# Performance work log

Measured on AMD Instinct MI355X. Metric: run time of the kernel, lower is better.

Reference implementation:

```python
import jax, jax.numpy as jnp
import numpy as np

K = 3
PAD = 1


def conv3x3(x, w):
    # x: [B,C,H,W], w: [O,C,3,3] -> [B,O,H,W], stride 1, pad 1, no bias
    return jax.lax.conv_general_dilated(
        x, w, window_strides=(1, 1), padding=((PAD, PAD), (PAD, PAD)),
        dimension_numbers=("NCHW", "OIHW", "NCHW"))


def bilinear_gather(x, py, px):
    """Zero-padded bilinear sampling (torchvision deform_conv2d semantics).
    x: [B,C,H,W]; py, px: [B,KK,H,W] absolute sampling coords.
    Returns [B,C,KK,H,W]."""
    B, C, H, W = x.shape
    KK = py.shape[1]
    y0 = jnp.floor(py)
    x0 = jnp.floor(px)
    wy1 = py - y0  # frac weights
    wx1 = px - x0
    wy0 = 1.0 - wy1
    wx0 = 1.0 - wx1
    x_flat = x.reshape(B, C, H * W)

    def corner(yi, xi, w):
        valid = (yi >= 0) & (yi <= H - 1) & (xi >= 0) & (xi <= W - 1)
        yc = jnp.clip(yi, 0, H - 1).astype(jnp.int32)
        xc = jnp.clip(xi, 0, W - 1).astype(jnp.int32)
        idx = (yc * W + xc).reshape(B, 1, KK * H * W)
        v = jnp.take_along_axis(x_flat, jnp.broadcast_to(idx, (B, C, KK * H * W)), axis=2)
        v = v.reshape(B, C, KK, H, W)
        return v * (w * valid.astype(x.dtype))[:, None]

    return (corner(y0, x0, wy0 * wx0) + corner(y0, x0 + 1.0, wy0 * wx1)
            + corner(y0 + 1.0, x0, wy1 * wx0) + corner(y0 + 1.0, x0 + 1.0, wy1 * wx1))


def deform_conv2d(x, offset, weight):
    """x: [B,C,H,W]; offset: [B,2*K*K,H,W] (dy,dx interleaved per tap, row-major);
    weight: [O,C,K,K]. stride 1, pad 1, dilation 1, 1 group, 1 offset group."""
    B, C, H, W = x.shape
    O = weight.shape[0]
    off = offset.reshape(B, K * K, 2, H, W)
    dy, dx = off[:, :, 0], off[:, :, 1]  # [B,9,H,W]
    ki, kj = jnp.meshgrid(jnp.arange(K, dtype=x.dtype), jnp.arange(K, dtype=x.dtype), indexing="ij")
    ki = ki.reshape(1, K * K, 1, 1)
    kj = kj.reshape(1, K * K, 1, 1)
    hh = jnp.arange(H, dtype=x.dtype).reshape(1, 1, H, 1)
    ww = jnp.arange(W, dtype=x.dtype).reshape(1, 1, 1, W)
    py = hh - PAD + ki + dy  # [B,9,H,W]
    px = ww - PAD + kj + dx
    sampled = bilinear_gather(x, py, px)  # [B,C,9,H,W]
    return jnp.einsum("bckhw,ock->bohw", sampled, weight.reshape(O, C, K * K))


def offset_estimator(x, w1, w2, w3):
    # channel-preserving bottleneck stand-in for Dynamic_offset_estimator
    h = jax.nn.relu(conv3x3(x, w1))
    h = jax.nn.relu(conv3x3(h, w2))
    return conv3x3(h, w3)


def setup_inputs() -> dict:
    key = jax.random.key(0)
    ks = jax.random.split(key, 7)
    B, C, H, W = 1, 768, 64, 64
    C2, CM = 2 * C, 192
    f32 = jnp.float32
    inp = {
        "input_features": jax.random.normal(ks[0], (B, C, H, W), dtype=f32),
        "reference_features": jax.random.normal(ks[1], (B, C, H, W), dtype=f32),
        "est_w1": jax.random.normal(ks[2], (CM, C2, K, K), dtype=f32) / np.sqrt(C2 * K * K),
        "est_w2": jax.random.normal(ks[3], (CM, CM, K, K), dtype=f32) / np.sqrt(CM * K * K),
        "est_w3": jax.random.normal(ks[4], (C2, CM, K, K), dtype=f32) / np.sqrt(CM * K * K),
        "offset_w": jax.random.normal(ks[5], (18, C2, K, K), dtype=f32) / np.sqrt(C2 * K * K),
        "deform_w": jax.random.normal(ks[6], (C, C, K, K), dtype=f32) / np.sqrt(C * K * K),
    }
    return inp


def reference(input_features, reference_features, est_w1, est_w2, est_w3, offset_w, deform_w):
    input_offset = jnp.concatenate([input_features, reference_features], axis=1)  # [B,2C,H,W]
    est = offset_estimator(input_offset, est_w1, est_w2, est_w3)  # [B,2C,H,W]
    offset = conv3x3(est, offset_w)  # [B,18,H,W]
    return deform_conv2d(reference_features, offset, deform_w)  # [B,C,H,W]
```

## Files before the change

kernel.cpp:

```cpp
#include <hip/hip_runtime.h>

#define HWPX 4096

typedef short s8v  __attribute__((ext_vector_type(8)));
typedef float f4v  __attribute__((ext_vector_type(4)));

__device__ inline unsigned short f2bf(float f) {
    unsigned u = __float_as_uint(f);
    return (unsigned short)((u + 0x7fffu + ((u >> 16) & 1u)) >> 16);
}
__device__ inline float bf2f(unsigned s) {
    return __uint_as_float(s << 16);
}

__global__ __launch_bounds__(256)
void tr_cat_k(const float* __restrict__ xa, const float* __restrict__ xb,
              short* __restrict__ xt)
{
    __shared__ __align__(16) short T[64 * 72];
    const int c0 = blockIdx.x * 64, p0 = blockIdx.y * 64, tid = threadIdx.x;
    for (int i = tid; i < 4096; i += 256) {
        int cl = i >> 6, pl = i & 63;
        int c = c0 + cl;
        float v = (c < 768) ? xa[(size_t)c * HWPX + p0 + pl]
                            : xb[(size_t)(c - 768) * HWPX + p0 + pl];
        T[pl * 72 + cl] = (short)f2bf(v);
    }
    __syncthreads();
    for (int i = tid; i < 512; i += 256) {
        int pl = i >> 3, part = i & 7;
        uint4 v = *(const uint4*)&T[pl * 72 + part * 8];
        *(uint4*)&xt[(size_t)(p0 + pl) * 1536 + c0 + part * 8] = v;
    }
}

__global__ __launch_bounds__(256)
void wpack_k(const float* __restrict__ src, short* __restrict__ dst,
             int Cin, int Cout, int S, int NB, int total)
{
    int i = blockIdx.x * 256 + threadIdx.x;
    if (i >= total) return;
    int e = i & 7, lane = (i >> 3) & 63;
    int lm = lane & 15, quad = lane >> 4;
    int rest = i >> 9;
    int f = rest % NB;
    int s = (rest / NB) % S;
    int g = rest / (NB * S);
    int cout = g * (NB * 16) + f * 16 + lm;
    int cb = s / 9, t = s % 9;
    int ch = cb * 32 + quad * 8 + e;
    dst[i] = (cout < Cout) ? (short)f2bf(src[((size_t)cout * Cin + ch) * 9 + t]) : 0;
}

__global__ __launch_bounds__(256, 4)
void convf_k(const short* __restrict__ Xt, int CinStr,
             const short* __restrict__ Wp, int S, int chunks,
             short* __restrict__ Out, int Cstr, int splitStride)
{
    __shared__ __align__(16) short sH[6 * 66 * 40];
    const int tid = threadIdx.x, lane = tid & 63, wv = tid >> 6;
    const int lm = lane & 15, quad = lane >> 4;
    const int r0 = blockIdx.x * 4;
    const int g  = blockIdx.y;
    const int cb0 = blockIdx.z * chunks;
    short* out = Out + (size_t)blockIdx.z * splitStride;

    f4v acc[4][2];
#pragma unroll
    for (int ma = 0; ma < 4; ++ma)
#pragma unroll
        for (int nb = 0; nb < 2; ++nb)
#pragma unroll
            for (int r = 0; r < 4; ++r) acc[ma][nb][r] = 0.f;

    for (int cc = 0; cc < chunks; ++cc) {
        const int cb = cb0 + cc;
        const short* wpB = Wp + ((size_t)(g * S + cb * 9) * 2) * 512 + lane * 8;
        s8v bb[2];
        bb[0] = *(const s8v*)&wpB[0];
        bb[1] = *(const s8v*)&wpB[512];

        for (int i = tid; i < 1584; i += 256) {
            int slot = i >> 2, part = i & 3;
            int hr = slot / 66, px = slot % 66;
            int gy = r0 - 1 + hr, gx = px - 1;
            uint4 v = {0, 0, 0, 0};
            if (gy >= 0 && gy < 64 && gx >= 0 && gx < 64)
                v = *(const uint4*)&Xt[(size_t)(gy * 64 + gx) * CinStr + cb * 32 + part * 8];
            *(uint4*)&sH[slot * 40 + part * 8] = v;
        }
        __syncthreads();

#pragma unroll
        for (int t = 0; t < 9; ++t) {
            const int ty = t / 3, tx = t % 3;
            s8v nb0 = *(const s8v*)&wpB[(size_t)((t + 1) * 2 + 0) * 512];
            s8v nb1 = *(const s8v*)&wpB[(size_t)((t + 1) * 2 + 1) * 512];
            s8v a[4];
#pragma unroll
            for (int ma = 0; ma < 4; ++ma)
                a[ma] = *(const s8v*)&sH[((wv + ty) * 66 + ma * 16 + lm + tx) * 40 + quad * 8];
#pragma unroll
            for (int ma = 0; ma < 4; ++ma) {
                acc[ma][0] = __builtin_amdgcn_mfma_f32_16x16x32_bf16(a[ma], bb[0], acc[ma][0], 0, 0, 0);
                acc[ma][1] = __builtin_amdgcn_mfma_f32_16x16x32_bf16(a[ma], bb[1], acc[ma][1], 0, 0, 0);
            }
            bb[0] = nb0; bb[1] = nb1;
        }
        __syncthreads();
    }

    const int py = (r0 + wv) * 64;
#pragma unroll
    for (int ma = 0; ma < 4; ++ma)
#pragma unroll
        for (int nb = 0; nb < 2; ++nb)
#pragma unroll
            for (int r = 0; r < 4; ++r)
                out[(size_t)(py + ma * 16 + quad * 4 + r) * Cstr + g * 32 + nb * 16 + lm]
                    = (short)f2bf(acc[ma][nb][r]);
}

__global__ __launch_bounds__(256)
void ep_sumb_k(const short* __restrict__ P, short* __restrict__ outb,
               int nsplit, size_t splitStride, int n8, int relu)
{
    int i = blockIdx.x * 256 + threadIdx.x;
    if (i >= n8) return;
    size_t base = (size_t)i * 8;
    float s[8];
#pragma unroll
    for (int j = 0; j < 8; ++j) s[j] = 0.f;
    for (int sp = 0; sp < nsplit; ++sp) {
        uint4 v = *(const uint4*)&P[sp * splitStride + base];
        s[0] += bf2f(v.x & 0xffffu); s[1] += bf2f(v.x >> 16);
        s[2] += bf2f(v.y & 0xffffu); s[3] += bf2f(v.y >> 16);
        s[4] += bf2f(v.z & 0xffffu); s[5] += bf2f(v.z >> 16);
        s[6] += bf2f(v.w & 0xffffu); s[7] += bf2f(v.w >> 16);
    }
    if (relu) {
#pragma unroll
        for (int j = 0; j < 8; ++j) s[j] = fmaxf(s[j], 0.f);
    }
    uint4 o;
    o.x = f2bf(s[0]) | ((unsigned)f2bf(s[1]) << 16);
    o.y = f2bf(s[2]) | ((unsigned)f2bf(s[3]) << 16);
    o.z = f2bf(s[4]) | ((unsigned)f2bf(s[5]) << 16);
    o.w = f2bf(s[6]) | ((unsigned)f2bf(s[7]) << 16);
    *(uint4*)&outb[base] = o;
}

__global__ __launch_bounds__(256)
void ep_offs_k(const short* __restrict__ P, float* __restrict__ offs)
{
    int i = blockIdx.x * 256 + threadIdx.x;
    if (i >= 18 * HWPX) return;
    int m = i >> 12, px = i & 4095;
    float s = 0.f;
    for (int sp = 0; sp < 16; ++sp)
        s += bf2f((unsigned short)P[((size_t)sp * HWPX + px) * 32 + m]);
    offs[i] = s;
}

__global__ __launch_bounds__(256)
void sample_k(const short* __restrict__ xcat, const float* __restrict__ offs,
              short* __restrict__ Smp)
{
    __shared__ int   s_mi[9][16][4];
    __shared__ float s_mw[9][16][4];
    const int tid = threadIdx.x;
    const int p0  = blockIdx.x * 16;
    const int gb  = blockIdx.y * 24;

    if (tid < 144) {
        int t = tid / 16, p = tid % 16;
        int pxg = p0 + p;
        int r = pxg >> 6, x = pxg & 63;
        float dy = offs[(size_t)(2 * t)     * HWPX + pxg];
        float dx = offs[(size_t)(2 * t + 1) * HWPX + pxg];
        float py  = (float)(r - 1 + t / 3) + dy;
        float pxf = (float)(x - 1 + t % 3) + dx;
        py  = fminf(fmaxf(py,  -1e6f), 1e6f);
        pxf = fminf(fmaxf(pxf, -1e6f), 1e6f);
        float y0f = floorf(py), x0f = floorf(pxf);
        float wy1 = py - y0f, wx1 = pxf - x0f;
        float wy0 = 1.f - wy1, wx0 = 1.f - wx1;
        bool vy0 = (y0f >=  0.f) && (y0f <= 63.f);
        bool vy1 = (y0f >= -1.f) && (y0f <= 62.f);
        bool vx0 = (x0f >=  0.f) && (x0f <= 63.f);
        bool vx1 = (x0f >= -1.f) && (x0f <= 62.f);
        int y0 = (int)fminf(fmaxf(y0f,       0.f), 63.f);
        int y1 = (int)fminf(fmaxf(y0f + 1.f, 0.f), 63.f);
        int x0 = (int)fminf(fmaxf(x0f,       0.f), 63.f);
        int x1 = (int)fminf(fmaxf(x0f + 1.f, 0.f), 63.f);
        s_mi[t][p][0] = y0 * 64 + x0;  s_mw[t][p][0] = (vy0 && vx0) ? wy0 * wx0 : 0.f;
        s_mi[t][p][1] = y0 * 64 + x1;  s_mw[t][p][1] = (vy0 && vx1) ? wy0 * wx1 : 0.f;
        s_mi[t][p][2] = y1 * 64 + x0;  s_mw[t][p][2] = (vy1 && vx0) ? wy1 * wx0 : 0.f;
        s_mi[t][p][3] = y1 * 64 + x1;  s_mw[t][p][3] = (vy1 && vx1) ? wy1 * wx1 : 0.f;
    }
    __syncthreads();

    for (int i = tid; i < 16 * 9 * 24; i += 256) {
        int p = i / 216, rest = i % 216;
        int t = rest / 24, g = gb + rest % 24;
        float a[8];
#pragma unroll
        for (int j = 0; j < 8; ++j) a[j] = 0.f;
#pragma unroll
        for (int c = 0; c < 4; ++c) {
            float w = s_mw[t][p][c];
            const short* src = xcat + (size_t)s_mi[t][p][c] * 1536 + 768 + g * 8;
            uint4 v = *(const uint4*)src;
            a[0] += w * bf2f(v.x & 0xffffu); a[1] += w * bf2f(v.x >> 16);
            a[2] += w * bf2f(v.y & 0xffffu); a[3] += w * bf2f(v.y >> 16);
            a[4] += w * bf2f(v.z & 0xffffu); a[5] += w * bf2f(v.z >> 16);
            a[6] += w * bf2f(v.w & 0xffffu); a[7] += w * bf2f(v.w >> 16);
        }
        uint4 o;
        o.x = f2bf(a[0]) | ((unsigned)f2bf(a[1]) << 16);
        o.y = f2bf(a[2]) | ((unsigned)f2bf(a[3]) << 16);
        o.z = f2bf(a[4]) | ((unsigned)f2bf(a[5]) << 16);
        o.w = f2bf(a[6]) | ((unsigned)f2bf(a[7]) << 16);
        int px = p0 + p;
        int pg = px >> 6, ma = (px >> 4) & 3, lmx = px & 15;
        int cb = g >> 2, qd = g & 3;
        size_t addr = ((((size_t)pg * 216 + cb * 9 + t) * 4 + ma) * 64 + qd * 16 + lmx) * 8;
        *(uint4*)&Smp[addr] = o;
    }
}

__global__ __launch_bounds__(256, 3)
void dgemm_k(const short* __restrict__ Ap, const short* __restrict__ Bp,
             short* __restrict__ P)
{
    const int tid = threadIdx.x, lane = tid & 63, wv = tid >> 6;
    const int lm = lane & 15, quad = lane >> 4;
    const int mg = blockIdx.y * 2 + (wv >> 1);
    const int pg = blockIdx.x * 2 + (wv & 1);
    const int s0 = blockIdx.z * 54;
    const short* ap = Ap + (((size_t)mg * 216 + s0) * 4 * 64 + lane) * 8;
    const short* bp = Bp + (((size_t)pg * 216 + s0) * 4 * 64 + lane) * 8;

    f4v acc[4][4];
#pragma unroll
    for (int ma = 0; ma < 4; ++ma)
#pragma unroll
        for (int nb = 0; nb < 4; ++nb)
#pragma unroll
            for (int r = 0; r < 4; ++r) acc[ma][nb][r] = 0.f;

    s8v a0[4], b0[4], a1[4], b1[4];
#pragma unroll
    for (int f = 0; f < 4; ++f) {
        a0[f] = *(const s8v*)&ap[(size_t)f * 512];
        b0[f] = *(const s8v*)&bp[(size_t)f * 512];
    }

    for (int s = 0; s < 54; s += 2) {
#pragma unroll
        for (int f = 0; f < 4; ++f) {
            a1[f] = *(const s8v*)&ap[(size_t)((s + 1) * 4 + f) * 512];
            b1[f] = *(const s8v*)&bp[(size_t)((s + 1) * 4 + f) * 512];
        }
#pragma unroll
        for (int ma = 0; ma < 4; ++ma)
#pragma unroll
            for (int nb = 0; nb < 4; ++nb)
                acc[ma][nb] = __builtin_amdgcn_mfma_f32_16x16x32_bf16(
                    a0[ma], b0[nb], acc[ma][nb], 0, 0, 0);
#pragma unroll
        for (int f = 0; f < 4; ++f) {
            a0[f] = *(const s8v*)&ap[(size_t)((s + 2) * 4 + f) * 512];
            b0[f] = *(const s8v*)&bp[(size_t)((s + 2) * 4 + f) * 512];
        }
#pragma unroll
        for (int ma = 0; ma < 4; ++ma)
#pragma unroll
            for (int nb = 0; nb < 4; ++nb)
                acc[ma][nb] = __builtin_amdgcn_mfma_f32_16x16x32_bf16(
                    a1[ma], b1[nb], acc[ma][nb], 0, 0, 0);
    }

    short* p = P + (size_t)blockIdx.z * 768 * HWPX;
#pragma unroll
    for (int ma = 0; ma < 4; ++ma)
#pragma unroll
        for (int nb = 0; nb < 4; ++nb)
#pragma unroll
            for (int r = 0; r < 4; ++r)
                p[(size_t)(mg * 64 + ma * 16 + quad * 4 + r) * HWPX
                  + pg * 64 + nb * 16 + lm] = (short)f2bf(acc[ma][nb][r]);
}

__global__ __launch_bounds__(256)
void ep_dg_k(const short* __restrict__ P, float* __restrict__ out)
{
    int i = blockIdx.x * 256 + threadIdx.x;
    if (i >= 768 * HWPX / 8) return;
    size_t base = (size_t)i * 8;
    float s[8];
#pragma unroll
    for (int j = 0; j < 8; ++j) s[j] = 0.f;
    for (int sp = 0; sp < 4; ++sp) {
        uint4 v = *(const uint4*)&P[(size_t)sp * 768 * HWPX + base];
        s[0] += bf2f(v.x & 0xffffu); s[1] += bf2f(v.x >> 16);
        s[2] += bf2f(v.y & 0xffffu); s[3] += bf2f(v.y >> 16);
        s[4] += bf2f(v.z & 0xffffu); s[5] += bf2f(v.z >> 16);
        s[6] += bf2f(v.w & 0xffffu); s[7] += bf2f(v.w >> 16);
    }
    float4 o0 = make_float4(s[0], s[1], s[2], s[3]);
    float4 o1 = make_float4(s[4], s[5], s[6], s[7]);
    *(float4*)&out[base]     = o0;
    *(float4*)&out[base + 4] = o1;
}

extern "C" void kernel_launch(void* const* d_in, const int* in_sizes, int n_in,
                              void* d_out, int out_size, void* d_ws, size_t ws_size,
                              hipStream_t stream)
{
    const float* x_in  = (const float*)d_in[0];
    const float* x_ref = (const float*)d_in[1];
    const float* w1    = (const float*)d_in[2];
    const float* w2    = (const float*)d_in[3];
    const float* w3    = (const float*)d_in[4];
    const float* ow    = (const float*)d_in[5];
    const float* dw    = (const float*)d_in[6];
    float* out = (float*)d_out;

    char* w = (char*)d_ws;
    size_t off = 0;
    auto carve = [&](size_t bytes) {
        void* p = w + off;
        off += (bytes + 255) & ~(size_t)255;
        return p;
    };
    short* xcat = (short*)carve((size_t)4096 * 1536 * 2);
    short* w1p  = (short*)carve((size_t)6 * 432 * 2 * 512 * 2);
    short* w2p  = (short*)carve((size_t)6 * 54 * 2 * 512 * 2);
    short* w3p  = (short*)carve((size_t)48 * 54 * 2 * 512 * 2);
    short* w4p  = (short*)carve((size_t)1 * 432 * 2 * 512 * 2);
    short* dwp  = (short*)carve((size_t)12 * 216 * 4 * 512 * 2);
    float* offs = (float*)carve((size_t)18 * 4096 * 4);
    short* Smp  = (short*)carve((size_t)4096 * 6912 * 2);
    char*  R    = (char*)carve((size_t)2 * 768 * 4096 * 4);
    short* rh1  = (short*)R;
    short* rh2  = (short*)(R + 1572864);
    short* Pb   = (short*)(R + 3145728);
    short* est  = (short*)(R + 3145728);
    short* Pb4  = (short*)(R + 15728640);
    short* Pdg  = (short*)R;

    tr_cat_k<<<dim3(24, 64), 256, 0, stream>>>(x_in, x_ref, xcat);
    {
        int t1 = 6 * 432 * 2 * 512;
        wpack_k<<<(t1 + 255) / 256, 256, 0, stream>>>(w1, w1p, 1536, 192, 432, 2, t1);
        int t2 = 6 * 54 * 2 * 512;
        wpack_k<<<(t2 + 255) / 256, 256, 0, stream>>>(w2, w2p, 192, 192, 54, 2, t2);
        int t3 = 48 * 54 * 2 * 512;
        wpack_k<<<(t3 + 255) / 256, 256, 0, stream>>>(w3, w3p, 192, 1536, 54, 2, t3);
        int t4 = 1 * 432 * 2 * 512;
        wpack_k<<<(t4 + 255) / 256, 256, 0, stream>>>(ow, w4p, 1536, 18, 432, 2, t4);
        int t5 = 12 * 216 * 4 * 512;
        wpack_k<<<(t5 + 255) / 256, 256, 0, stream>>>(dw, dwp, 768, 768, 216, 4, t5);
    }

    const int n8 = 4096 * 192 / 8;
    convf_k<<<dim3(16, 6, 12), 256, 0, stream>>>(xcat, 1536, w1p, 432, 4,
                                                 Pb, 192, 4096 * 192);
    ep_sumb_k<<<(n8 + 255) / 256, 256, 0, stream>>>(Pb, rh1, 12, (size_t)4096 * 192, n8, 1);
    convf_k<<<dim3(16, 6, 6), 256, 0, stream>>>(rh1, 192, w2p, 54, 1,
                                                Pb, 192, 4096 * 192);
    ep_sumb_k<<<(n8 + 255) / 256, 256, 0, stream>>>(Pb, rh2, 6, (size_t)4096 * 192, n8, 1);
    convf_k<<<dim3(16, 48, 1), 256, 0, stream>>>(rh2, 192, w3p, 54, 6,
                                                 est, 1536, 0);
    convf_k<<<dim3(16, 1, 16), 256, 0, stream>>>(est, 1536, w4p, 432, 3,
                                                 Pb4, 32, 4096 * 32);
    ep_offs_k<<<(18 * HWPX + 255) / 256, 256, 0, stream>>>(Pb4, offs);
    sample_k<<<dim3(256, 4), 256, 0, stream>>>(xcat, offs, Smp);
    dgemm_k<<<dim3(32, 6, 4), 256, 0, stream>>>(dwp, Smp, Pdg);
    ep_dg_k<<<(768 * HWPX / 8 + 255) / 256, 256, 0, stream>>>(Pdg, out);
}
```

Before: 355.5 us.

## Widen conv output tile to 64 channels, retune split-K, fuse weight packing

Templates the conv kernel on the number of 16-wide output-channel blocks and uses 4 blocks (64 channels) for the estimator convs, so each staged input halo tile in LDS is reused across more MFMAs. Split-K factors and grids are retuned per layer, conv3 becomes split-K with an extra reduction pass, and the offset conv is split 48 ways. The five weight-packing launches are merged into one kernel and the partial buffers move into the sampling workspace. The cost is more accumulator registers, which lowers the launch-bounds occupancy hint from 4 to 3, plus extra partial-sum traffic for conv3.

```diff
diff --git a/kernel.cpp b/kernel.cpp
--- a/kernel.cpp
+++ b/kernel.cpp
@@ -34,12 +34,9 @@
     }
 }
 
-__global__ __launch_bounds__(256)
-void wpack_k(const float* __restrict__ src, short* __restrict__ dst,
-             int Cin, int Cout, int S, int NB, int total)
-{
-    int i = blockIdx.x * 256 + threadIdx.x;
-    if (i >= total) return;
+__device__ inline void wpack1(const float* __restrict__ src, short* __restrict__ dst,
+                              int i, int Cin, int Cout, int S, int NB)
+{
     int e = i & 7, lane = (i >> 3) & 63;
     int lm = lane & 15, quad = lane >> 4;
     int rest = i >> 9;
@@ -52,7 +49,30 @@
     dst[i] = (cout < Cout) ? (short)f2bf(src[((size_t)cout * Cin + ch) * 9 + t]) : 0;
 }
 
-__global__ __launch_bounds__(256, 4)
+#define C1 2654208
+#define C2 2985984
+#define C3 5640192
+#define C4 6082560
+#define C5 11390976
+
+__global__ __launch_bounds__(256)
+void wpack_all_k(const float* __restrict__ s1, const float* __restrict__ s2,
+                 const float* __restrict__ s3, const float* __restrict__ s4,
+                 const float* __restrict__ s5,
+                 short* __restrict__ d1, short* __restrict__ d2,
+                 short* __restrict__ d3, short* __restrict__ d4,
+                 short* __restrict__ d5)
+{
+    int i = blockIdx.x * 256 + threadIdx.x;
+    if (i < C1)      wpack1(s1, d1, i,      1536, 192,  432, 4);
+    else if (i < C2) wpack1(s2, d2, i - C1, 192,  192,  54,  4);
+    else if (i < C3) wpack1(s3, d3, i - C2, 192,  1536, 54,  4);
+    else if (i < C4) wpack1(s4, d4, i - C3, 1536, 18,   432, 2);
+    else if (i < C5) wpack1(s5, d5, i - C4, 768,  768,  216, 4);
+}
+
+template<int NB>
+__global__ __launch_bounds__(256, 3)
 void convf_k(const short* __restrict__ Xt, int CinStr,
              const short* __restrict__ Wp, int S, int chunks,
              short* __restrict__ Out, int Cstr, int splitStride)
@@ -65,20 +85,21 @@
     const int cb0 = blockIdx.z * chunks;
     short* out = Out + (size_t)blockIdx.z * splitStride;
 
-    f4v acc[4][2];
+    f4v acc[4][NB];
 #pragma unroll
     for (int ma = 0; ma < 4; ++ma)
 #pragma unroll
-        for (int nb = 0; nb < 2; ++nb)
+        for (int nb = 0; nb < NB; ++nb)
 #pragma unroll
             for (int r = 0; r < 4; ++r) acc[ma][nb][r] = 0.f;
 
     for (int cc = 0; cc < chunks; ++cc) {
         const int cb = cb0 + cc;
-        const short* wpB = Wp + ((size_t)(g * S + cb * 9) * 2) * 512 + lane * 8;
-        s8v bb[2];
-        bb[0] = *(const s8v*)&wpB[0];
-        bb[1] = *(const s8v*)&wpB[512];
+        const short* wpB = Wp + ((size_t)(g * S + cb * 9) * NB) * 512 + lane * 8;
+        s8v bb[NB];
+#pragma unroll
+        for (int f = 0; f < NB; ++f)
+            bb[f] = *(const s8v*)&wpB[(size_t)f * 512];
 
         for (int i = tid; i < 1584; i += 256) {
             int slot = i >> 2, part = i & 3;
@@ -94,18 +115,22 @@
 #pragma unroll
         for (int t = 0; t < 9; ++t) {
             const int ty = t / 3, tx = t % 3;
-            s8v nb0 = *(const s8v*)&wpB[(size_t)((t + 1) * 2 + 0) * 512];
-            s8v nb1 = *(const s8v*)&wpB[(size_t)((t + 1) * 2 + 1) * 512];
+            s8v nxt[NB];
+#pragma unroll
+            for (int f = 0; f < NB; ++f)
+                nxt[f] = *(const s8v*)&wpB[(size_t)((t + 1) * NB + f) * 512];
             s8v a[4];
 #pragma unroll
             for (int ma = 0; ma < 4; ++ma)
                 a[ma] = *(const s8v*)&sH[((wv + ty) * 66 + ma * 16 + lm + tx) * 40 + quad * 8];
 #pragma unroll
-            for (int ma = 0; ma < 4; ++ma) {
-                acc[ma][0] = __builtin_amdgcn_mfma_f32_16x16x32_bf16(a[ma], bb[0], acc[ma][0], 0, 0, 0);
-                acc[ma][1] = __builtin_amdgcn_mfma_f32_16x16x32_bf16(a[ma], bb[1], acc[ma][1], 0, 0, 0);
-            }
-            bb[0] = nb0; bb[1] = nb1;
+            for (int ma = 0; ma < 4; ++ma)
+#pragma unroll
+                for (int nb = 0; nb < NB; ++nb)
+                    acc[ma][nb] = __builtin_amdgcn_mfma_f32_16x16x32_bf16(
+                        a[ma], bb[nb], acc[ma][nb], 0, 0, 0);
+#pragma unroll
+            for (int f = 0; f < NB; ++f) bb[f] = nxt[f];
         }
         __syncthreads();
     }
@@ -114,11 +139,11 @@
 #pragma unroll
     for (int ma = 0; ma < 4; ++ma)
 #pragma unroll
-        for (int nb = 0; nb < 2; ++nb)
+        for (int nb = 0; nb < NB; ++nb)
 #pragma unroll
             for (int r = 0; r < 4; ++r)
-                out[(size_t)(py + ma * 16 + quad * 4 + r) * Cstr + g * 32 + nb * 16 + lm]
-                    = (short)f2bf(acc[ma][nb][r]);
+                out[(size_t)(py + ma * 16 + quad * 4 + r) * Cstr
+                    + g * (NB * 16) + nb * 16 + lm] = (short)f2bf(acc[ma][nb][r]);
 }
 
 __global__ __launch_bounds__(256)
@@ -151,13 +176,13 @@
 }
 
 __global__ __launch_bounds__(256)
-void ep_offs_k(const short* __restrict__ P, float* __restrict__ offs)
+void ep_offs_k(const short* __restrict__ P, float* __restrict__ offs, int nsplit)
 {
     int i = blockIdx.x * 256 + threadIdx.x;
     if (i >= 18 * HWPX) return;
     int m = i >> 12, px = i & 4095;
     float s = 0.f;
-    for (int sp = 0; sp < 16; ++sp)
+    for (int sp = 0; sp < nsplit; ++sp)
         s += bf2f((unsigned short)P[((size_t)sp * HWPX + px) * 32 + m]);
     offs[i] = s;
 }
@@ -335,47 +360,40 @@
         return p;
     };
     short* xcat = (short*)carve((size_t)4096 * 1536 * 2);
-    short* w1p  = (short*)carve((size_t)6 * 432 * 2 * 512 * 2);
-    short* w2p  = (short*)carve((size_t)6 * 54 * 2 * 512 * 2);
-    short* w3p  = (short*)carve((size_t)48 * 54 * 2 * 512 * 2);
-    short* w4p  = (short*)carve((size_t)1 * 432 * 2 * 512 * 2);
-    short* dwp  = (short*)carve((size_t)12 * 216 * 4 * 512 * 2);
+    short* w1p  = (short*)carve((size_t)C1 * 2);
+    short* w2p  = (short*)carve((size_t)(C2 - C1) * 2);
+    short* w3p  = (short*)carve((size_t)(C3 - C2) * 2);
+    short* w4p  = (short*)carve((size_t)(C4 - C3) * 2);
+    short* dwp  = (short*)carve((size_t)(C5 - C4) * 2);
     float* offs = (float*)carve((size_t)18 * 4096 * 4);
     short* Smp  = (short*)carve((size_t)4096 * 6912 * 2);
     char*  R    = (char*)carve((size_t)2 * 768 * 4096 * 4);
     short* rh1  = (short*)R;
     short* rh2  = (short*)(R + 1572864);
-    short* Pb   = (short*)(R + 3145728);
     short* est  = (short*)(R + 3145728);
-    short* Pb4  = (short*)(R + 15728640);
+    short* Pcv  = Smp;
     short* Pdg  = (short*)R;
 
     tr_cat_k<<<dim3(24, 64), 256, 0, stream>>>(x_in, x_ref, xcat);
+    wpack_all_k<<<(C5 + 255) / 256, 256, 0, stream>>>(w1, w2, w3, ow, dw,
+                                                      w1p, w2p, w3p, w4p, dwp);
+
+    const int n8 = 4096 * 192 / 8;
+    convf_k<4><<<dim3(16, 3, 16), 256, 0, stream>>>(xcat, 1536, w1p, 432, 3,
+                                                    Pcv, 192, 4096 * 192);
+    ep_sumb_k<<<(n8 + 255) / 256, 256, 0, stream>>>(Pcv, rh1, 16, (size_t)4096 * 192, n8, 1);
+    convf_k<4><<<dim3(16, 3, 6), 256, 0, stream>>>(rh1, 192, w2p, 54, 1,
+                                                   Pcv, 192, 4096 * 192);
+    ep_sumb_k<<<(n8 + 255) / 256, 256, 0, stream>>>(Pcv, rh2, 6, (size_t)4096 * 192, n8, 1);
+    convf_k<4><<<dim3(16, 24, 2), 256, 0, stream>>>(rh2, 192, w3p, 54, 3,
+                                                    Pcv, 1536, 4096 * 1536);
     {
-        int t1 = 6 * 432 * 2 * 512;
-        wpack_k<<<(t1 + 255) / 256, 256, 0, stream>>>(w1, w1p, 1536, 192, 432, 2, t1);
-        int t2 = 6 * 54 * 2 * 512;
-        wpack_k<<<(t2 + 255) / 256, 256, 0, stream>>>(w2, w2p, 192, 192, 54, 2, t2);
-        int t3 = 48 * 54 * 2 * 512;
-        wpack_k<<<(t3 + 255) / 256, 256, 0, stream>>>(w3, w3p, 192, 1536, 54, 2, t3);
-        int t4 = 1 * 432 * 2 * 512;
-        wpack_k<<<(t4 + 255) / 256, 256, 0, stream>>>(ow, w4p, 1536, 18, 432, 2, t4);
-        int t5 = 12 * 216 * 4 * 512;
-        wpack_k<<<(t5 + 255) / 256, 256, 0, stream>>>(dw, dwp, 768, 768, 216, 4, t5);
-    }
-
-    const int n8 = 4096 * 192 / 8;
-    convf_k<<<dim3(16, 6, 12), 256, 0, stream>>>(xcat, 1536, w1p, 432, 4,
-                                                 Pb, 192, 4096 * 192);
-    ep_sumb_k<<<(n8 + 255) / 256, 256, 0, stream>>>(Pb, rh1, 12, (size_t)4096 * 192, n8, 1);
-    convf_k<<<dim3(16, 6, 6), 256, 0, stream>>>(rh1, 192, w2p, 54, 1,
-                                                Pb, 192, 4096 * 192);
-    ep_sumb_k<<<(n8 + 255) / 256, 256, 0, stream>>>(Pb, rh2, 6, (size_t)4096 * 192, n8, 1);
-    convf_k<<<dim3(16, 48, 1), 256, 0, stream>>>(rh2, 192, w3p, 54, 6,
-                                                 est, 1536, 0);
-    convf_k<<<dim3(16, 1, 16), 256, 0, stream>>>(est, 1536, w4p, 432, 3,
-                                                 Pb4, 32, 4096 * 32);
-    ep_offs_k<<<(18 * HWPX + 255) / 256, 256, 0, stream>>>(Pb4, offs);
+        const int n8c3 = 4096 * 1536 / 8;
+        ep_sumb_k<<<(n8c3 + 255) / 256, 256, 0, stream>>>(Pcv, est, 2, (size_t)4096 * 1536, n8c3, 0);
+    }
+    convf_k<2><<<dim3(16, 1, 48), 256, 0, stream>>>(est, 1536, w4p, 432, 1,
+                                                    Pcv, 32, 4096 * 32);
+    ep_offs_k<<<(18 * HWPX + 255) / 256, 256, 0, stream>>>(Pcv, offs, 48);
     sample_k<<<dim3(256, 4), 256, 0, stream>>>(xcat, offs, Smp);
     dgemm_k<<<dim3(32, 6, 4), 256, 0, stream>>>(dwp, Smp, Pdg);
     ep_dg_k<<<(768 * HWPX / 8 + 255) / 256, 256, 0, stream>>>(Pdg, out);
```

New measurement: 353.5 us. About the same (-0.6%).
